# Optimization experiments

Hardware: AMD Instinct MI355X
Metric: run time of the kernel (lower is better)

The kernel has to match this reference:

```python
import jax, jax.numpy as jnp
import numpy as np

D_MODEL = 1024
N_HEADS = 16
D_K = D_MODEL // N_HEADS


def setup_inputs() -> dict:
    key = jax.random.key(0)
    ks = jax.random.split(key, 9)
    s = 1.0 / np.sqrt(D_MODEL)
    x = jax.random.normal(ks[0], (2, 2048, D_MODEL), dtype=jnp.float32)
    Wq = jax.random.normal(ks[1], (D_MODEL, D_MODEL), dtype=jnp.float32) * s
    bq = jnp.zeros((D_MODEL,), jnp.float32)
    Wk = jax.random.normal(ks[2], (D_MODEL, D_MODEL), dtype=jnp.float32) * s
    bk = jnp.zeros((D_MODEL,), jnp.float32)
    Wv = jax.random.normal(ks[3], (D_MODEL, D_MODEL), dtype=jnp.float32) * s
    bv = jnp.zeros((D_MODEL,), jnp.float32)
    Wo = jax.random.normal(ks[4], (D_MODEL, D_MODEL), dtype=jnp.float32) * s
    bo = jnp.zeros((D_MODEL,), jnp.float32)
    return {"x": x, "Wq": Wq, "bq": bq, "Wk": Wk, "bk": bk,
            "Wv": Wv, "bv": bv, "Wo": Wo, "bo": bo}


def reference(x, Wq, bq, Wk, bk, Wv, bv, Wo, bo):
    B, T, C = x.shape
    H, Dk = N_HEADS, D_K
    # QKV projections, reshape to [B, H, T, Dk]
    q = (x @ Wq + bq).reshape(B, T, H, Dk).transpose(0, 2, 1, 3)
    k = (x @ Wk + bk).reshape(B, T, H, Dk).transpose(0, 2, 1, 3)
    v = (x @ Wv + bv).reshape(B, T, H, Dk).transpose(0, 2, 1, 3)
    scale = 1.0 / np.sqrt(Dk).astype(np.float32)
    att = jnp.einsum('bhqd,bhkd->bhqk', q, k) * scale  # [B,H,T,T]
    causal = jnp.tril(jnp.ones((T, T), dtype=bool))
    att = jnp.where(causal, att, -jnp.inf)
    att = jax.nn.softmax(att, axis=-1)
    y = jnp.einsum('bhqk,bhkd->bhqd', att, v)  # [B,H,T,Dk]
    y = y.transpose(0, 2, 1, 3).reshape(B, T, C)
    return y @ Wo + bo
```

## Files before the change

kernel.cpp:

```cpp
#include <hip/hip_runtime.h>
#include <stdint.h>

#define D_MODEL 1024
#define N_HEADS 16
#define D_K     64
#define T_SEQ   2048
#define BATCH   2
#define M_TOT   (BATCH * T_SEQ)
#define QCH     128

typedef __attribute__((ext_vector_type(8))) short  short8;
typedef __attribute__((ext_vector_type(4))) float  f32x4;
typedef __attribute__((ext_vector_type(4))) unsigned short u16x4;

typedef __attribute__((address_space(1))) void gvoid;
typedef __attribute__((address_space(3))) void lvoid;

#define QSCALE 0.18033688011112042f

static __device__ __forceinline__ unsigned short f2bf(float f) {
    union { float f; unsigned u; } v; v.f = f;
    unsigned u = v.u;
    u += 0x7fffu + ((u >> 16) & 1u);
    return (unsigned short)(u >> 16);
}
static __device__ __forceinline__ float bf2f(unsigned short s) {
    union { unsigned u; float f; } v; v.u = ((unsigned)s) << 16;
    return v.f;
}
static __device__ __forceinline__ float fexp2(float x) {
    float r;
    asm("v_exp_f32 %0, %1" : "=v"(r) : "v"(x));
    return r;
}
static __device__ __forceinline__ unsigned cvt_pk_bf16(float lo, float hi) {
    unsigned r;
    asm("v_cvt_pk_bf16_f32 %0, %1, %2" : "=v"(r) : "v"(lo), "v"(hi));
    return r;
}

__global__ void cvt_x(const float* __restrict__ in, unsigned short* __restrict__ out) {
    int idx = blockIdx.x * blockDim.x + threadIdx.x;
    const float4* in4 = (const float4*)in;
    float4 v = in4[idx];
    u16x4 o;
    o.x = f2bf(v.x); o.y = f2bf(v.y); o.z = f2bf(v.z); o.w = f2bf(v.w);
    *(u16x4*)&out[(size_t)idx * 4] = o;
}

__global__ void cvt_w_t(const float* w0, const float* w1, const float* w2, const float* w3,
                        unsigned short* o0, unsigned short* o1, unsigned short* o2, unsigned short* o3) {
    const float* w; unsigned short* o;
    switch (blockIdx.z) {
        case 0: w = w0; o = o0; break;
        case 1: w = w1; o = o1; break;
        case 2: w = w2; o = o2; break;
        default: w = w3; o = o3; break;
    }
    __shared__ float tile[32][33];
    int n0 = blockIdx.x * 32, k0 = blockIdx.y * 32;
    int tx = threadIdx.x, ty = threadIdx.y;
    #pragma unroll
    for (int r = 0; r < 32; r += 8)
        tile[ty + r][tx] = w[(size_t)(k0 + ty + r) * D_MODEL + n0 + tx];
    __syncthreads();
    #pragma unroll
    for (int r = 0; r < 32; r += 8)
        o[(size_t)(n0 + ty + r) * D_MODEL + k0 + tx] = f2bf(tile[tx][ty + r]);
}

__global__ __launch_bounds__(256) void gemm_qkv(const unsigned short* __restrict__ A,
                                                const unsigned short* __restrict__ wq,
                                                const unsigned short* __restrict__ wk,
                                                const unsigned short* __restrict__ wv,
                                                const float* __restrict__ bq,
                                                const float* __restrict__ bk,
                                                const float* __restrict__ bv,
                                                unsigned short* __restrict__ qo,
                                                unsigned short* __restrict__ ko,
                                                unsigned short* __restrict__ vo) {
    const int nb   = (blockIdx.x & 7) * 96 + (blockIdx.x >> 3);
    const int tn   = nb & 7;
    const int rest = nb >> 3;
    const int tm   = rest & 31;
    const int z    = rest >> 5;

    const unsigned short* Bt = (z == 0) ? wq : (z == 1) ? wk : wv;
    const float* bias = (z == 0) ? bq : (z == 1) ? bk : bv;
    const float alpha = (z == 0) ? QSCALE : 1.0f;

    __shared__ unsigned short lA[128 * 32];
    __shared__ unsigned short lB[128 * 32];
    const int tid  = threadIdx.x;
    const int w    = tid >> 6, lane = tid & 63;
    const int wm   = w & 1, wn = w >> 1;
    const int i16  = lane & 15, g4 = lane >> 4;
    f32x4 acc[4][4] = {};

    const int rA0 = tm * 128, rB0 = tn * 128;
    const int srow = lane >> 2;
    const int skc  = (lane & 3) * 8;

    for (int k0 = 0; k0 < D_MODEL; k0 += 32) {
        #pragma unroll
        for (int is = 0; is < 2; ++is) {
            int c   = is * 4 + w;
            int row = c * 16 + srow;
            __builtin_amdgcn_global_load_lds(
                (gvoid*)(A + (size_t)(rA0 + row) * D_MODEL + k0 + skc),
                (lvoid*)&lA[c * 512], 16, 0, 0);
            __builtin_amdgcn_global_load_lds(
                (gvoid*)(Bt + (size_t)(rB0 + row) * D_MODEL + k0 + skc),
                (lvoid*)&lB[c * 512], 16, 0, 0);
        }
        __syncthreads();
        short8 af[4], bfr[4];
        #pragma unroll
        for (int mi = 0; mi < 4; ++mi)
            af[mi] = *(const short8*)&lA[(wm * 64 + mi * 16 + i16) * 32 + g4 * 8];
        #pragma unroll
        for (int ni = 0; ni < 4; ++ni)
            bfr[ni] = *(const short8*)&lB[(wn * 64 + ni * 16 + i16) * 32 + g4 * 8];
        #pragma unroll
        for (int mi = 0; mi < 4; ++mi)
            #pragma unroll
            for (int ni = 0; ni < 4; ++ni)
                acc[mi][ni] = __builtin_amdgcn_mfma_f32_16x16x32_bf16(af[mi], bfr[ni], acc[mi][ni], 0, 0, 0);
        __syncthreads();
    }

    #pragma unroll
    for (int mi = 0; mi < 4; ++mi)
        #pragma unroll
        for (int ni = 0; ni < 4; ++ni) {
            int col = tn * 128 + wn * 64 + ni * 16 + i16;
            float bv2 = bias[col];
            #pragma unroll
            for (int r = 0; r < 4; ++r) {
                int row = tm * 128 + wm * 64 + mi * 16 + g4 * 4 + r;
                float val = (acc[mi][ni][r] + bv2) * alpha;
                int b = row >> 11, t = row & (T_SEQ - 1);
                int h = col >> 6,  d = col & (D_K - 1);
                unsigned short bfv = f2bf(val);
                if (z == 2)
                    vo[(((size_t)(b * N_HEADS + h)) * D_K + d) * T_SEQ + t] = bfv;
                else if (z == 1)
                    ko[(((size_t)(b * N_HEADS + h)) * T_SEQ + t) * D_K + d] = bfv;
                else
                    qo[(((size_t)(b * N_HEADS + h)) * T_SEQ + t) * D_K + d] = bfv;
            }
        }
}

__global__ __launch_bounds__(256) void gemm_out(const unsigned short* __restrict__ A,
                                                const unsigned short* __restrict__ Bt,
                                                const float* __restrict__ bias,
                                                float* __restrict__ Cout) {
    const int nb = (blockIdx.x & 7) * 32 + (blockIdx.x >> 3);
    const int tn = nb & 7;
    const int tm = nb >> 3;

    __shared__ unsigned short lA[128 * 32];
    __shared__ unsigned short lB[128 * 32];
    const int tid  = threadIdx.x;
    const int w    = tid >> 6, lane = tid & 63;
    const int wm   = w & 1, wn = w >> 1;
    const int i16  = lane & 15, g4 = lane >> 4;
    f32x4 acc[4][4] = {};

    const int rA0 = tm * 128, rB0 = tn * 128;
    const int srow = lane >> 2;
    const int skc  = (lane & 3) * 8;

    for (int k0 = 0; k0 < D_MODEL; k0 += 32) {
        #pragma unroll
        for (int is = 0; is < 2; ++is) {
            int c   = is * 4 + w;
            int row = c * 16 + srow;
            __builtin_amdgcn_global_load_lds(
                (gvoid*)(A + (size_t)(rA0 + row) * D_MODEL + k0 + skc),
                (lvoid*)&lA[c * 512], 16, 0, 0);
            __builtin_amdgcn_global_load_lds(
                (gvoid*)(Bt + (size_t)(rB0 + row) * D_MODEL + k0 + skc),
                (lvoid*)&lB[c * 512], 16, 0, 0);
        }
        __syncthreads();
        short8 af[4], bfr[4];
        #pragma unroll
        for (int mi = 0; mi < 4; ++mi)
            af[mi] = *(const short8*)&lA[(wm * 64 + mi * 16 + i16) * 32 + g4 * 8];
        #pragma unroll
        for (int ni = 0; ni < 4; ++ni)
            bfr[ni] = *(const short8*)&lB[(wn * 64 + ni * 16 + i16) * 32 + g4 * 8];
        #pragma unroll
        for (int mi = 0; mi < 4; ++mi)
            #pragma unroll
            for (int ni = 0; ni < 4; ++ni)
                acc[mi][ni] = __builtin_amdgcn_mfma_f32_16x16x32_bf16(af[mi], bfr[ni], acc[mi][ni], 0, 0, 0);
        __syncthreads();
    }

    #pragma unroll
    for (int mi = 0; mi < 4; ++mi)
        #pragma unroll
        for (int ni = 0; ni < 4; ++ni) {
            int col = tn * 128 + wn * 64 + ni * 16 + i16;
            float bv2 = bias[col];
            #pragma unroll
            for (int r = 0; r < 4; ++r) {
                int row = tm * 128 + wm * 64 + mi * 16 + g4 * 4 + r;
                Cout[(size_t)row * D_MODEL + col] = acc[mi][ni][r] + bv2;
            }
        }
}

__global__ __launch_bounds__(512, 4) void flash5(const unsigned short* __restrict__ q,
                                                 const unsigned short* __restrict__ k,
                                                 const unsigned short* __restrict__ vt,
                                                 unsigned short* __restrict__ opart,
                                                 float* __restrict__ lws) {
    __shared__ unsigned short lK[2][64 * 64];
    __shared__ unsigned short lV[2][64 * 64];
    __shared__ unsigned short lP[8][16 * 64];
    const int tid  = threadIdx.x;
    const int w    = tid >> 6, lane = tid & 63;
    const int i16  = lane & 15, g4 = lane >> 4;
    const int l8   = lane & 7,  g8 = lane >> 3;

    const int nb = (blockIdx.x & 7) * 64 + (blockIdx.x >> 3);
    const int p  = nb & 7;
    const int h  = (nb >> 3) & 1;
    const int bh = nb >> 4;
    const int w4 = w & 3;
    const int c  = (w >> 2) ? p : (15 - p);
    const int q0w = c * QCH + w4 * 32;
    const int cnt = 16 - p;

    const unsigned short* kp = k  + (size_t)bh * T_SEQ * D_K;
    const unsigned short* vp = vt + (size_t)bh * D_K * T_SEQ;
    const unsigned short* qp = q  + ((size_t)bh * T_SEQ + q0w) * D_K;
    unsigned short* Pw = &lP[w][0];
    const int swz = (i16 & 7) << 3;

    const int srow = tid >> 3;
    const int sco  = (l8 ^ g8) << 3;

    short8 qf[2][2];
    #pragma unroll
    for (int qt = 0; qt < 2; ++qt)
        #pragma unroll
        for (int ks = 0; ks < 2; ++ks)
            qf[qt][ks] = *(const short8*)&qp[(qt * 16 + i16) * D_K + ks * 32 + g4 * 8];

    f32x4 o[2][4] = {};
    float l[2] = {0.f, 0.f};

    auto stage = [&](int buf, int kv0s) {
        __builtin_amdgcn_global_load_lds(
            (gvoid*)(kp + (size_t)(kv0s + srow) * D_K + sco),
            (lvoid*)&lK[buf][(size_t)tid * 8], 16, 0, 0);
        __builtin_amdgcn_global_load_lds(
            (gvoid*)(vp + (size_t)srow * T_SEQ + kv0s + sco),
            (lvoid*)&lV[buf][(size_t)tid * 8], 16, 0, 0);
    };

    stage(0, h * 64);
    __syncthreads();

    for (int it = 0; it < cnt; ++it) {
        const int cur = it & 1;
        const int kv0 = (h + 2 * it) * 64;
        if (it + 1 < cnt) stage(cur ^ 1, kv0 + 128);

        if (kv0 <= q0w + 31) {
            const bool act0 = (kv0 <= q0w + 15);
            const unsigned short* Kc = &lK[cur][0];
            const unsigned short* Vc = &lV[cur][0];

            f32x4 s[4][2] = {};
            __builtin_amdgcn_s_setprio(1);
            #pragma unroll
            for (int ks = 0; ks < 2; ++ks)
                #pragma unroll
                for (int kt = 0; kt < 4; ++kt) {
                    short8 ka = *(const short8*)&Kc[(kt * 16 + i16) * 64 + ((ks * 32 + g4 * 8) ^ swz)];
                    if (act0)
                        s[kt][0] = __builtin_amdgcn_mfma_f32_16x16x32_bf16(ka, qf[0][ks], s[kt][0], 0, 0, 0);
                    s[kt][1] = __builtin_amdgcn_mfma_f32_16x16x32_bf16(ka, qf[1][ks], s[kt][1], 0, 0, 0);
                }
            __builtin_amdgcn_s_setprio(0);

            #pragma unroll
            for (int qt = 0; qt < 2; ++qt) {
                if (qt == 0 && !act0) continue;
                const int qrow = q0w + qt * 16 + i16;
                const bool diag = (kv0 + 63 > q0w + qt * 16);
                float ps = 0.f;
                unsigned pk[8];
                #pragma unroll
                for (int kt = 0; kt < 4; ++kt) {
                    f32x4 sc = s[kt][qt];
                    if (diag) {
                        #pragma unroll
                        for (int r = 0; r < 4; ++r)
                            if (kv0 + kt * 16 + g4 * 4 + r > qrow) sc[r] = -3e38f;
                    }
                    float p0 = fexp2(sc[0]), p1 = fexp2(sc[1]);
                    float p2 = fexp2(sc[2]), p3 = fexp2(sc[3]);
                    ps += (p0 + p1) + (p2 + p3);
                    pk[kt * 2]     = cvt_pk_bf16(p0, p1);
                    pk[kt * 2 + 1] = cvt_pk_bf16(p2, p3);
                }
                l[qt] += ps;
                #pragma unroll
                for (int kt = 0; kt < 4; ++kt) {
                    uint2 v2; v2.x = pk[kt * 2]; v2.y = pk[kt * 2 + 1];
                    *(uint2*)&Pw[i16 * 64 + ((kt * 16 + g4 * 4) ^ swz)] = v2;
                }
                short8 pB0 = *(const short8*)&Pw[i16 * 64 + (( 0 + g4 * 8) ^ swz)];
                short8 pB1 = *(const short8*)&Pw[i16 * 64 + ((32 + g4 * 8) ^ swz)];
                __builtin_amdgcn_s_setprio(1);
                #pragma unroll
                for (int dt = 0; dt < 4; ++dt) {
                    short8 va0 = *(const short8*)&Vc[(dt * 16 + i16) * 64 + (( 0 + g4 * 8) ^ swz)];
                    short8 va1 = *(const short8*)&Vc[(dt * 16 + i16) * 64 + ((32 + g4 * 8) ^ swz)];
                    o[qt][dt] = __builtin_amdgcn_mfma_f32_16x16x32_bf16(va0, pB0, o[qt][dt], 0, 0, 0);
                    o[qt][dt] = __builtin_amdgcn_mfma_f32_16x16x32_bf16(va1, pB1, o[qt][dt], 0, 0, 0);
                }
                __builtin_amdgcn_s_setprio(0);
            }
        }
        __syncthreads();
    }

    const int b = bh >> 4, hh = bh & 15;
    unsigned short* op = opart + (size_t)h * ((size_t)M_TOT * D_MODEL);
    #pragma unroll
    for (int qt = 0; qt < 2; ++qt) {
        float lt = l[qt] + __shfl_xor(l[qt], 16);
        lt += __shfl_xor(lt, 32);
        const int trow = q0w + qt * 16 + i16;
        if (g4 == 0)
            lws[((size_t)h * 32 + bh) * T_SEQ + trow] = lt;
        #pragma unroll
        for (int dt = 0; dt < 4; ++dt) {
            u16x4 ov;
            ov.x = f2bf(o[qt][dt][0]);
            ov.y = f2bf(o[qt][dt][1]);
            ov.z = f2bf(o[qt][dt][2]);
            ov.w = f2bf(o[qt][dt][3]);
            *(u16x4*)&op[((size_t)(b * T_SEQ) + trow) * D_MODEL + hh * D_K + dt * 16 + g4 * 4] = ov;
        }
    }
}

__global__ __launch_bounds__(256) void merge_halves(const unsigned short* __restrict__ op,
                                                    const float* __restrict__ lws,
                                                    unsigned short* __restrict__ y) {
    const int idx = blockIdx.x * 256 + threadIdx.x;
    const int gl  = idx * 8;
    const int row = gl >> 10;
    const int col = gl & 1023;
    const int b = row >> 11, t = row & (T_SEQ - 1), h = col >> 6;
    const float l0 = lws[((size_t)(b * 16 + h)) * T_SEQ + t];
    const float l1 = lws[((size_t)(32 + b * 16 + h)) * T_SEQ + t];
    const float inv = 1.0f / (l0 + l1);
    short8 a = *(const short8*)&op[gl];
    short8 cc = *(const short8*)&op[(size_t)M_TOT * D_MODEL + gl];
    short8 r;
    #pragma unroll
    for (int j = 0; j < 8; ++j) {
        float f = bf2f((unsigned short)a[j]) + bf2f((unsigned short)cc[j]);
        r[j] = (short)f2bf(f * inv);
    }
    *(short8*)&y[gl] = r;
}

extern "C" void kernel_launch(void* const* d_in, const int* in_sizes, int n_in,
                              void* d_out, int out_size, void* d_ws, size_t ws_size,
                              hipStream_t stream) {
    const float* x  = (const float*)d_in[0];
    const float* Wq = (const float*)d_in[1];
    const float* bq = (const float*)d_in[2];
    const float* Wk = (const float*)d_in[3];
    const float* bk = (const float*)d_in[4];
    const float* Wv = (const float*)d_in[5];
    const float* bv = (const float*)d_in[6];
    const float* Wo = (const float*)d_in[7];
    const float* bo = (const float*)d_in[8];

    uint8_t* ws = (uint8_t*)d_ws;
    const size_t MB = (size_t)1 << 20;
    unsigned short* xb  = (unsigned short*)(ws);
    unsigned short* wqt = (unsigned short*)(ws + 8  * MB);
    unsigned short* wkt = (unsigned short*)(ws + 10 * MB);
    unsigned short* wvt = (unsigned short*)(ws + 12 * MB);
    unsigned short* wot = (unsigned short*)(ws + 14 * MB);
    unsigned short* qb  = (unsigned short*)(ws + 16 * MB);
    unsigned short* kb  = (unsigned short*)(ws + 24 * MB);
    unsigned short* vtb = (unsigned short*)(ws + 32 * MB);
    float* lws = (float*)(ws + 8 * MB);

    cvt_x<<<4096, 256, 0, stream>>>(x, xb);
    cvt_w_t<<<dim3(32, 32, 4), dim3(32, 8), 0, stream>>>(Wq, Wk, Wv, Wo, wqt, wkt, wvt, wot);

    gemm_qkv<<<768, 256, 0, stream>>>(xb, wqt, wkt, wvt, bq, bk, bv, qb, kb, vtb);

    flash5<<<512, 512, 0, stream>>>(qb, kb, vtb, (unsigned short*)d_out, lws);
    merge_halves<<<2048, 256, 0, stream>>>((const unsigned short*)d_out, lws, xb);

    gemm_out<<<256, 256, 0, stream>>>(xb, wot, bo, (float*)d_out);
}
```

Before: 129.2 us.

## Split causal attention KV range three ways with 256-thread blocks and 3-way merge

The flash kernel now splits each head's KV blocks across three interleaved partitions instead of two, using 256-thread blocks that process two query chunks sequentially (a long and a short one for balance), giving 768 blocks. The merge kernel combines three partial outputs and denominators, reusing the x buffer and q buffer as scratch. The GEMM kernels drop their swizzled block-index remapping in favour of plain 2D/3D grids. This trades more partial-output traffic and merge work for better load balance and occupancy in attention, and may lose the L2 locality the previous block ordering provided.

```diff
diff --git a/kernel.cpp b/kernel.cpp
--- a/kernel.cpp
+++ b/kernel.cpp
@@ -79,12 +79,7 @@
                                                 unsigned short* __restrict__ qo,
                                                 unsigned short* __restrict__ ko,
                                                 unsigned short* __restrict__ vo) {
-    const int nb   = (blockIdx.x & 7) * 96 + (blockIdx.x >> 3);
-    const int tn   = nb & 7;
-    const int rest = nb >> 3;
-    const int tm   = rest & 31;
-    const int z    = rest >> 5;
-
+    const int z = blockIdx.z;
     const unsigned short* Bt = (z == 0) ? wq : (z == 1) ? wk : wv;
     const float* bias = (z == 0) ? bq : (z == 1) ? bk : bv;
     const float alpha = (z == 0) ? QSCALE : 1.0f;
@@ -93,6 +88,7 @@
     __shared__ unsigned short lB[128 * 32];
     const int tid  = threadIdx.x;
     const int w    = tid >> 6, lane = tid & 63;
+    const int tm   = blockIdx.y, tn = blockIdx.x;
     const int wm   = w & 1, wn = w >> 1;
     const int i16  = lane & 15, g4 = lane >> 4;
     f32x4 acc[4][4] = {};
@@ -156,14 +152,11 @@
                                                 const unsigned short* __restrict__ Bt,
                                                 const float* __restrict__ bias,
                                                 float* __restrict__ Cout) {
-    const int nb = (blockIdx.x & 7) * 32 + (blockIdx.x >> 3);
-    const int tn = nb & 7;
-    const int tm = nb >> 3;
-
     __shared__ unsigned short lA[128 * 32];
     __shared__ unsigned short lB[128 * 32];
     const int tid  = threadIdx.x;
     const int w    = tid >> 6, lane = tid & 63;
+    const int tm   = blockIdx.y, tn = blockIdx.x;
     const int wm   = w & 1, wn = w >> 1;
     const int i16  = lane & 15, g4 = lane >> 4;
     f32x4 acc[4][4] = {};
@@ -214,163 +207,175 @@
         }
 }
 
-__global__ __launch_bounds__(512, 4) void flash5(const unsigned short* __restrict__ q,
+__global__ __launch_bounds__(256, 3) void flash6(const unsigned short* __restrict__ q,
                                                  const unsigned short* __restrict__ k,
                                                  const unsigned short* __restrict__ vt,
-                                                 unsigned short* __restrict__ opart,
+                                                 unsigned short* __restrict__ op01,
+                                                 unsigned short* __restrict__ op2,
                                                  float* __restrict__ lws) {
     __shared__ unsigned short lK[2][64 * 64];
     __shared__ unsigned short lV[2][64 * 64];
-    __shared__ unsigned short lP[8][16 * 64];
+    __shared__ unsigned short lP[4][16 * 64];
     const int tid  = threadIdx.x;
     const int w    = tid >> 6, lane = tid & 63;
     const int i16  = lane & 15, g4 = lane >> 4;
     const int l8   = lane & 7,  g8 = lane >> 3;
-
-    const int nb = (blockIdx.x & 7) * 64 + (blockIdx.x >> 3);
-    const int p  = nb & 7;
-    const int h  = (nb >> 3) & 1;
-    const int bh = nb >> 4;
-    const int w4 = w & 3;
-    const int c  = (w >> 2) ? p : (15 - p);
-    const int q0w = c * QCH + w4 * 32;
-    const int cnt = 16 - p;
+    const int nb   = blockIdx.x;
+    const int p    = nb & 7;
+    const int s    = (nb >> 3) % 3;
+    const int bh   = nb / 24;
 
     const unsigned short* kp = k  + (size_t)bh * T_SEQ * D_K;
     const unsigned short* vp = vt + (size_t)bh * D_K * T_SEQ;
-    const unsigned short* qp = q  + ((size_t)bh * T_SEQ + q0w) * D_K;
     unsigned short* Pw = &lP[w][0];
-    const int swz = (i16 & 7) << 3;
-
-    const int srow = tid >> 3;
-    const int sco  = (l8 ^ g8) << 3;
-
-    short8 qf[2][2];
-    #pragma unroll
-    for (int qt = 0; qt < 2; ++qt)
-        #pragma unroll
-        for (int ks = 0; ks < 2; ++ks)
-            qf[qt][ks] = *(const short8*)&qp[(qt * 16 + i16) * D_K + ks * 32 + g4 * 8];
-
-    f32x4 o[2][4] = {};
-    float l[2] = {0.f, 0.f};
+    const int swz  = (i16 & 7) << 3;
+    const int csrc = (l8 ^ g8) << 3;
+
+    const int b = bh >> 4, hh = bh & 15;
+    unsigned short* op = (s == 2) ? op2 : op01 + (size_t)s * ((size_t)M_TOT * D_MODEL);
 
     auto stage = [&](int buf, int kv0s) {
-        __builtin_amdgcn_global_load_lds(
-            (gvoid*)(kp + (size_t)(kv0s + srow) * D_K + sco),
-            (lvoid*)&lK[buf][(size_t)tid * 8], 16, 0, 0);
-        __builtin_amdgcn_global_load_lds(
-            (gvoid*)(vp + (size_t)srow * T_SEQ + kv0s + sco),
-            (lvoid*)&lV[buf][(size_t)tid * 8], 16, 0, 0);
+        #pragma unroll
+        for (int i = 0; i < 2; ++i) {
+            const int cidx = w * 2 + i;
+            const int row  = cidx * 8 + g8;
+            __builtin_amdgcn_global_load_lds(
+                (gvoid*)(kp + (size_t)(kv0s + row) * D_K + csrc),
+                (lvoid*)&lK[buf][cidx * 512], 16, 0, 0);
+            __builtin_amdgcn_global_load_lds(
+                (gvoid*)(vp + (size_t)row * T_SEQ + kv0s + csrc),
+                (lvoid*)&lV[buf][cidx * 512], 16, 0, 0);
+        }
     };
 
-    stage(0, h * 64);
-    __syncthreads();
-
-    for (int it = 0; it < cnt; ++it) {
-        const int cur = it & 1;
-        const int kv0 = (h + 2 * it) * 64;
-        if (it + 1 < cnt) stage(cur ^ 1, kv0 + 128);
-
-        if (kv0 <= q0w + 31) {
-            const bool act0 = (kv0 <= q0w + 15);
-            const unsigned short* Kc = &lK[cur][0];
-            const unsigned short* Vc = &lV[cur][0];
-
-            f32x4 s[4][2] = {};
-            __builtin_amdgcn_s_setprio(1);
+    #pragma unroll 1
+    for (int ci = 0; ci < 2; ++ci) {
+        const int c   = ci ? p : (15 - p);
+        const int q0w = c * QCH + w * 32;
+        const int cnt = (2 * c + 1 >= s) ? (2 * c + 1 - s) / 3 + 1 : 0;
+
+        const unsigned short* qp = q + ((size_t)bh * T_SEQ + q0w) * D_K;
+        short8 qf[2][2];
+        #pragma unroll
+        for (int qt = 0; qt < 2; ++qt)
             #pragma unroll
             for (int ks = 0; ks < 2; ++ks)
-                #pragma unroll
-                for (int kt = 0; kt < 4; ++kt) {
-                    short8 ka = *(const short8*)&Kc[(kt * 16 + i16) * 64 + ((ks * 32 + g4 * 8) ^ swz)];
-                    if (act0)
-                        s[kt][0] = __builtin_amdgcn_mfma_f32_16x16x32_bf16(ka, qf[0][ks], s[kt][0], 0, 0, 0);
-                    s[kt][1] = __builtin_amdgcn_mfma_f32_16x16x32_bf16(ka, qf[1][ks], s[kt][1], 0, 0, 0);
-                }
-            __builtin_amdgcn_s_setprio(0);
-
-            #pragma unroll
-            for (int qt = 0; qt < 2; ++qt) {
-                if (qt == 0 && !act0) continue;
-                const int qrow = q0w + qt * 16 + i16;
-                const bool diag = (kv0 + 63 > q0w + qt * 16);
-                float ps = 0.f;
-                unsigned pk[8];
-                #pragma unroll
-                for (int kt = 0; kt < 4; ++kt) {
-                    f32x4 sc = s[kt][qt];
-                    if (diag) {
-                        #pragma unroll
-                        for (int r = 0; r < 4; ++r)
-                            if (kv0 + kt * 16 + g4 * 4 + r > qrow) sc[r] = -3e38f;
-                    }
-                    float p0 = fexp2(sc[0]), p1 = fexp2(sc[1]);
-                    float p2 = fexp2(sc[2]), p3 = fexp2(sc[3]);
-                    ps += (p0 + p1) + (p2 + p3);
-                    pk[kt * 2]     = cvt_pk_bf16(p0, p1);
-                    pk[kt * 2 + 1] = cvt_pk_bf16(p2, p3);
-                }
-                l[qt] += ps;
-                #pragma unroll
-                for (int kt = 0; kt < 4; ++kt) {
-                    uint2 v2; v2.x = pk[kt * 2]; v2.y = pk[kt * 2 + 1];
-                    *(uint2*)&Pw[i16 * 64 + ((kt * 16 + g4 * 4) ^ swz)] = v2;
-                }
-                short8 pB0 = *(const short8*)&Pw[i16 * 64 + (( 0 + g4 * 8) ^ swz)];
-                short8 pB1 = *(const short8*)&Pw[i16 * 64 + ((32 + g4 * 8) ^ swz)];
+                qf[qt][ks] = *(const short8*)&qp[(qt * 16 + i16) * D_K + ks * 32 + g4 * 8];
+
+        f32x4 o[2][4] = {};
+        float l[2] = {0.f, 0.f};
+
+        if (cnt > 0) stage(0, s * 64);
+        __syncthreads();
+
+        for (int it = 0; it < cnt; ++it) {
+            const int cur = it & 1;
+            const int kv0 = (s + 3 * it) * 64;
+            if (it + 1 < cnt) stage(cur ^ 1, kv0 + 192);
+
+            if (kv0 <= q0w + 31) {
+                const bool act0 = (kv0 <= q0w + 15);
+                const unsigned short* Kc = &lK[cur][0];
+                const unsigned short* Vc = &lV[cur][0];
+
+                f32x4 sA[4][2] = {};
                 __builtin_amdgcn_s_setprio(1);
                 #pragma unroll
-                for (int dt = 0; dt < 4; ++dt) {
-                    short8 va0 = *(const short8*)&Vc[(dt * 16 + i16) * 64 + (( 0 + g4 * 8) ^ swz)];
-                    short8 va1 = *(const short8*)&Vc[(dt * 16 + i16) * 64 + ((32 + g4 * 8) ^ swz)];
-                    o[qt][dt] = __builtin_amdgcn_mfma_f32_16x16x32_bf16(va0, pB0, o[qt][dt], 0, 0, 0);
-                    o[qt][dt] = __builtin_amdgcn_mfma_f32_16x16x32_bf16(va1, pB1, o[qt][dt], 0, 0, 0);
+                for (int ks = 0; ks < 2; ++ks)
+                    #pragma unroll
+                    for (int kt = 0; kt < 4; ++kt) {
+                        short8 ka = *(const short8*)&Kc[(kt * 16 + i16) * 64 + ((ks * 32 + g4 * 8) ^ swz)];
+                        if (act0)
+                            sA[kt][0] = __builtin_amdgcn_mfma_f32_16x16x32_bf16(ka, qf[0][ks], sA[kt][0], 0, 0, 0);
+                        sA[kt][1] = __builtin_amdgcn_mfma_f32_16x16x32_bf16(ka, qf[1][ks], sA[kt][1], 0, 0, 0);
+                    }
+                __builtin_amdgcn_s_setprio(0);
+
+                #pragma unroll
+                for (int qt = 0; qt < 2; ++qt) {
+                    if (qt == 0 && !act0) continue;
+                    const int qrow = q0w + qt * 16 + i16;
+                    const bool diag = (kv0 + 63 > q0w + qt * 16);
+                    float ps = 0.f;
+                    unsigned pk[8];
+                    #pragma unroll
+                    for (int kt = 0; kt < 4; ++kt) {
+                        f32x4 sc = sA[kt][qt];
+                        if (diag) {
+                            #pragma unroll
+                            for (int r = 0; r < 4; ++r)
+                                if (kv0 + kt * 16 + g4 * 4 + r > qrow) sc[r] = -3e38f;
+                        }
+                        float p0 = fexp2(sc[0]), p1 = fexp2(sc[1]);
+                        float p2 = fexp2(sc[2]), p3 = fexp2(sc[3]);
+                        ps += (p0 + p1) + (p2 + p3);
+                        pk[kt * 2]     = cvt_pk_bf16(p0, p1);
+                        pk[kt * 2 + 1] = cvt_pk_bf16(p2, p3);
+                    }
+                    l[qt] += ps;
+                    #pragma unroll
+                    for (int kt = 0; kt < 4; ++kt) {
+                        uint2 v2; v2.x = pk[kt * 2]; v2.y = pk[kt * 2 + 1];
+                        *(uint2*)&Pw[i16 * 64 + ((kt * 16 + g4 * 4) ^ swz)] = v2;
+                    }
+                    short8 pB0 = *(const short8*)&Pw[i16 * 64 + (( 0 + g4 * 8) ^ swz)];
+                    short8 pB1 = *(const short8*)&Pw[i16 * 64 + ((32 + g4 * 8) ^ swz)];
+                    __builtin_amdgcn_s_setprio(1);
+                    #pragma unroll
+                    for (int dt = 0; dt < 4; ++dt) {
+                        short8 va0 = *(const short8*)&Vc[(dt * 16 + i16) * 64 + (( 0 + g4 * 8) ^ swz)];
+                        short8 va1 = *(const short8*)&Vc[(dt * 16 + i16) * 64 + ((32 + g4 * 8) ^ swz)];
+                        o[qt][dt] = __builtin_amdgcn_mfma_f32_16x16x32_bf16(va0, pB0, o[qt][dt], 0, 0, 0);
+                        o[qt][dt] = __builtin_amdgcn_mfma_f32_16x16x32_bf16(va1, pB1, o[qt][dt], 0, 0, 0);
+                    }
+                    __builtin_amdgcn_s_setprio(0);
                 }
-                __builtin_amdgcn_s_setprio(0);
             }
+            __syncthreads();
+        }
+
+        #pragma unroll
+        for (int qt = 0; qt < 2; ++qt) {
+            float lt = l[qt] + __shfl_xor(l[qt], 16);
+            lt += __shfl_xor(lt, 32);
+            const int trow = q0w + qt * 16 + i16;
+            if (g4 == 0)
+                lws[((size_t)s * 32 + bh) * T_SEQ + trow] = lt;
+            #pragma unroll
+            for (int dt = 0; dt < 4; ++dt) {
+                u16x4 ov;
+                ov.x = f2bf(o[qt][dt][0]);
+                ov.y = f2bf(o[qt][dt][1]);
+                ov.z = f2bf(o[qt][dt][2]);
+                ov.w = f2bf(o[qt][dt][3]);
+                *(u16x4*)&op[((size_t)(b * T_SEQ) + trow) * D_MODEL + hh * D_K + dt * 16 + g4 * 4] = ov;
+            }
         }
         __syncthreads();
     }
-
-    const int b = bh >> 4, hh = bh & 15;
-    unsigned short* op = opart + (size_t)h * ((size_t)M_TOT * D_MODEL);
-    #pragma unroll
-    for (int qt = 0; qt < 2; ++qt) {
-        float lt = l[qt] + __shfl_xor(l[qt], 16);
-        lt += __shfl_xor(lt, 32);
-        const int trow = q0w + qt * 16 + i16;
-        if (g4 == 0)
-            lws[((size_t)h * 32 + bh) * T_SEQ + trow] = lt;
-        #pragma unroll
-        for (int dt = 0; dt < 4; ++dt) {
-            u16x4 ov;
-            ov.x = f2bf(o[qt][dt][0]);
-            ov.y = f2bf(o[qt][dt][1]);
-            ov.z = f2bf(o[qt][dt][2]);
-            ov.w = f2bf(o[qt][dt][3]);
-            *(u16x4*)&op[((size_t)(b * T_SEQ) + trow) * D_MODEL + hh * D_K + dt * 16 + g4 * 4] = ov;
-        }
-    }
-}
-
-__global__ __launch_bounds__(256) void merge_halves(const unsigned short* __restrict__ op,
-                                                    const float* __restrict__ lws,
-                                                    unsigned short* __restrict__ y) {
+}
+
+__global__ __launch_bounds__(256) void merge3(const unsigned short* __restrict__ op01,
+                                              const unsigned short* __restrict__ op2,
+                                              const float* __restrict__ lws,
+                                              unsigned short* __restrict__ y) {
     const int idx = blockIdx.x * 256 + threadIdx.x;
     const int gl  = idx * 8;
     const int row = gl >> 10;
     const int col = gl & 1023;
     const int b = row >> 11, t = row & (T_SEQ - 1), h = col >> 6;
-    const float l0 = lws[((size_t)(b * 16 + h)) * T_SEQ + t];
-    const float l1 = lws[((size_t)(32 + b * 16 + h)) * T_SEQ + t];
-    const float inv = 1.0f / (l0 + l1);
-    short8 a = *(const short8*)&op[gl];
-    short8 cc = *(const short8*)&op[(size_t)M_TOT * D_MODEL + gl];
+    const int bh = b * 16 + h;
+    const float l0 = lws[((size_t)bh) * T_SEQ + t];
+    const float l1 = lws[((size_t)(32 + bh)) * T_SEQ + t];
+    const float l2 = lws[((size_t)(64 + bh)) * T_SEQ + t];
+    const float inv = 1.0f / (l0 + l1 + l2);
+    short8 a0 = *(const short8*)&op01[gl];
+    short8 a1 = *(const short8*)&op01[(size_t)M_TOT * D_MODEL + gl];
+    short8 a2 = *(const short8*)&op2[gl];
     short8 r;
     #pragma unroll
     for (int j = 0; j < 8; ++j) {
-        float f = bf2f((unsigned short)a[j]) + bf2f((unsigned short)cc[j]);
+        float f = bf2f((unsigned short)a0[j]) + bf2f((unsigned short)a1[j]) + bf2f((unsigned short)a2[j]);
         r[j] = (short)f2bf(f * inv);
     }
     *(short8*)&y[gl] = r;
@@ -404,10 +409,10 @@
     cvt_x<<<4096, 256, 0, stream>>>(x, xb);
     cvt_w_t<<<dim3(32, 32, 4), dim3(32, 8), 0, stream>>>(Wq, Wk, Wv, Wo, wqt, wkt, wvt, wot);
 
-    gemm_qkv<<<768, 256, 0, stream>>>(xb, wqt, wkt, wvt, bq, bk, bv, qb, kb, vtb);
-
-    flash5<<<512, 512, 0, stream>>>(qb, kb, vtb, (unsigned short*)d_out, lws);
-    merge_halves<<<2048, 256, 0, stream>>>((const unsigned short*)d_out, lws, xb);
-
-    gemm_out<<<256, 256, 0, stream>>>(xb, wot, bo, (float*)d_out);
-}
+    gemm_qkv<<<dim3(8, 32, 3), 256, 0, stream>>>(xb, wqt, wkt, wvt, bq, bk, bv, qb, kb, vtb);
+
+    flash6<<<768, 256, 0, stream>>>(qb, kb, vtb, (unsigned short*)d_out, xb, lws);
+    merge3<<<2048, 256, 0, stream>>>((const unsigned short*)d_out, xb, lws, qb);
+
+    gemm_out<<<dim3(8, 32), 256, 0, stream>>>(qb, wot, bo, (float*)d_out);
+}
```

Result: faster. 120.8 us (-6.5%).
